# Optimization experiments

Hardware: AMD Instinct MI355X
Metric: run time of the kernel (lower is better)

Reference implementation:

```python
import jax, jax.numpy as jnp
import numpy as np

B, IN, H = 4096, 1024, 1024


def setup_inputs() -> dict:
    key = jax.random.key(0)
    ks = jax.random.split(key, 16)
    s_in = 1.0 / np.sqrt(IN)
    s_h = 1.0 / np.sqrt(H)
    d = {
        "x_t": jax.random.normal(ks[0], (B, IN), jnp.float32),
        "h_prev": jax.random.normal(ks[1], (B, H), jnp.float32),
        "c_prev": jax.random.normal(ks[2], (B, H), jnp.float32),
    }
    # input->hidden weights (with bias), stored torch-style as (out, in)
    for i, name in enumerate(["ii", "if", "ig", "io"]):
        d[f"W_{name}"] = jax.random.uniform(ks[3 + i], (H, IN), jnp.float32, -s_in, s_in)
        d[f"b_{name}"] = jax.random.uniform(ks[7 + i], (H,), jnp.float32, -s_in, s_in)
    # hidden->hidden weights (no bias)
    for i, name in enumerate(["hi", "hf", "hg", "ho"]):
        d[f"W_{name}"] = jax.random.uniform(ks[11 + i], (H, H), jnp.float32, -s_h, s_h)
    return d


def reference(x_t, h_prev, c_prev,
              W_ii, b_ii, W_if, b_if, W_ig, b_ig, W_io, b_io,
              W_hi, W_hf, W_hg, W_ho):
    # Fuse the 8 small GEMMs into 2 concatenated GEMMs (same math).
    Wx = jnp.concatenate([W_ii, W_if, W_ig, W_io], axis=0)   # (4H, IN)
    Wh = jnp.concatenate([W_hi, W_hf, W_hg, W_ho], axis=0)   # (4H, H)
    b = jnp.concatenate([b_ii, b_if, b_ig, b_io], axis=0)    # (4H,)
    gates = x_t @ Wx.T + h_prev @ Wh.T + b                    # (B, 4H)
    zi, zf, zg, zo = jnp.split(gates, 4, axis=1)
    i_t = jax.nn.sigmoid(zi)
    f_t = jax.nn.sigmoid(zf)
    g_t = jnp.tanh(zg)
    o_t = jax.nn.sigmoid(zo)
    c_t = f_t * c_prev + i_t * g_t
    h_t = o_t * jnp.tanh(c_t)
    return (h_t, c_t, (i_t, f_t, g_t, o_t))
```

## Files before the change

### kernel.cpp

```cpp
#include <hip/hip_runtime.h>
#include <hip/hip_bf16.h>

#define B_DIM 4096
#define K_TOT 2048
#define H_DIM 1024

typedef short bf16x8 __attribute__((ext_vector_type(8)));
typedef float f32x4 __attribute__((ext_vector_type(4)));
typedef unsigned short u16x8 __attribute__((ext_vector_type(8)));

typedef __attribute__((address_space(1))) const unsigned gas_u32;
typedef __attribute__((address_space(3))) unsigned las_u32;

static __device__ __forceinline__ unsigned short f2bf(float f) {
  union { float f; unsigned u; } v; v.f = f;
  unsigned r = v.u + 0x7FFF + ((v.u >> 16) & 1);
  return (unsigned short)(r >> 16);
}

__global__ void pack_a(const float* __restrict__ x, const float* __restrict__ hp,
                       u16x8* __restrict__ A) {
  int t = blockIdx.x * blockDim.x + threadIdx.x;
  int idx = t << 3;
  int b = idx >> 11;
  int k = idx & 2047;
  const float* src = (k < 1024) ? (x + b * 1024 + k) : (hp + b * 1024 + (k - 1024));
  float4 lo = *(const float4*)src;
  float4 hi = *(const float4*)(src + 4);
  u16x8 v;
  v[0] = f2bf(lo.x); v[1] = f2bf(lo.y); v[2] = f2bf(lo.z); v[3] = f2bf(lo.w);
  v[4] = f2bf(hi.x); v[5] = f2bf(hi.y); v[6] = f2bf(hi.z); v[7] = f2bf(hi.w);
  A[t] = v;
}

__global__ void pack_w(const float* __restrict__ W0, const float* __restrict__ W1,
                       const float* __restrict__ W2, const float* __restrict__ W3,
                       const float* __restrict__ W4, const float* __restrict__ W5,
                       const float* __restrict__ W6, const float* __restrict__ W7,
                       u16x8* __restrict__ Wc) {
  int t = blockIdx.x * blockDim.x + threadIdx.x;
  int idx = t << 3;
  int n = idx >> 11;
  int k = idx & 2047;
  int gate = n >> 10;
  int j = n & 1023;
  int s = (k < 1024) ? gate : gate + 4;
  const float* base =
      (s == 0) ? W0 : (s == 1) ? W1 : (s == 2) ? W2 : (s == 3) ? W3 :
      (s == 4) ? W4 : (s == 5) ? W5 : (s == 6) ? W6 : W7;
  const float* src = base + j * 1024 + (k & 1023);
  float4 lo = *(const float4*)src;
  float4 hi = *(const float4*)(src + 4);
  u16x8 v;
  v[0] = f2bf(lo.x); v[1] = f2bf(lo.y); v[2] = f2bf(lo.z); v[3] = f2bf(lo.w);
  v[4] = f2bf(hi.x); v[5] = f2bf(hi.y); v[6] = f2bf(hi.z); v[7] = f2bf(hi.w);
  Wc[t] = v;
}

static __device__ __forceinline__ float sigm(float x) {
  return 1.0f / (1.0f + __expf(-x));
}
static __device__ __forceinline__ float tanh_fast(float x) {
  x = fminf(fmaxf(x, -15.f), 15.f);
  float t = __expf(-2.0f * x);
  return (1.0f - t) / (1.0f + t);
}

__global__ __launch_bounds__(256) void gemm_lstm(
    const unsigned short* __restrict__ A,
    const unsigned short* __restrict__ W,
    const float* __restrict__ cp,
    const float* __restrict__ bii, const float* __restrict__ bif,
    const float* __restrict__ big, const float* __restrict__ bio,
    float* __restrict__ out) {
  __shared__ unsigned short As[128 * 32];
  __shared__ unsigned short Bs[128 * 32];
  const int tid = threadIdx.x;
  const int wave = tid >> 6;
  const int lane = tid & 63;
  const int m0 = blockIdx.y << 7;
  const int j0 = blockIdx.x << 5;
  const int wm = (wave >> 1) << 6;
  const int wj16 = (wave & 1) << 4;

  f32x4 acc[4][4];
#pragma unroll
  for (int mi = 0; mi < 4; ++mi)
#pragma unroll
    for (int ni = 0; ni < 4; ++ni)
      acc[mi][ni] = (f32x4){0.f, 0.f, 0.f, 0.f};

  const int c0 = wave * 2;
  const int lr = lane >> 2;
  const int ls = lane & 3;
  const int g  = ls ^ ((lr >> 1) & 3);
  const unsigned short* aptr0 = A + (long)(m0 + c0 * 16 + lr) * K_TOT + g * 8;
  const unsigned short* aptr1 = A + (long)(m0 + (c0 + 1) * 16 + lr) * K_TOT + g * 8;
  const int rr0 = c0 * 16 + lr;
  const int rr1 = rr0 + 16;
  const unsigned short* bptr0 =
      W + (long)((rr0 >> 5) * 1024 + j0 + (rr0 & 31)) * K_TOT + g * 8;
  const unsigned short* bptr1 =
      W + (long)((rr1 >> 5) * 1024 + j0 + (rr1 & 31)) * K_TOT + g * 8;
  char* lA0 = (char*)As + c0 * 1024;
  char* lA1 = lA0 + 1024;
  char* lB0 = (char*)Bs + c0 * 1024;
  char* lB1 = lB0 + 1024;

  const int fr = lane & 15;
  const int gg = lane >> 4;
  const int sl = (gg ^ ((fr >> 1) & 3)) * 16;

  for (int k0 = 0; k0 < K_TOT; k0 += 32) {
    __builtin_amdgcn_global_load_lds((gas_u32*)(aptr0 + k0), (las_u32*)lA0, 16, 0, 0);
    __builtin_amdgcn_global_load_lds((gas_u32*)(aptr1 + k0), (las_u32*)lA1, 16, 0, 0);
    __builtin_amdgcn_global_load_lds((gas_u32*)(bptr0 + k0), (las_u32*)lB0, 16, 0, 0);
    __builtin_amdgcn_global_load_lds((gas_u32*)(bptr1 + k0), (las_u32*)lB1, 16, 0, 0);
    __syncthreads();
    bf16x8 af[4], bfv[4];
#pragma unroll
    for (int i = 0; i < 4; ++i) {
      af[i]  = *(const bf16x8*)((const char*)As + (wm + i * 16 + fr) * 64 + sl);
      bfv[i] = *(const bf16x8*)((const char*)Bs + (i * 32 + wj16 + fr) * 64 + sl);
    }
#pragma unroll
    for (int mi = 0; mi < 4; ++mi)
#pragma unroll
      for (int ni = 0; ni < 4; ++ni)
        acc[mi][ni] = __builtin_amdgcn_mfma_f32_16x16x32_bf16(af[mi], bfv[ni], acc[mi][ni], 0, 0, 0);
    __syncthreads();
  }

  const int ccol = lane & 15;
  const int crow = (lane >> 4) * 4;
  const int j = j0 + wj16 + ccol;
  const float bi = bii[j];
  const float bff = bif[j];
  const float bg = big[j];
  const float bo = bio[j];
  const long BH = (long)B_DIM * H_DIM;
#pragma unroll
  for (int mi = 0; mi < 4; ++mi) {
#pragma unroll
    for (int reg = 0; reg < 4; ++reg) {
      const int row = m0 + wm + mi * 16 + crow + reg;
      const long p = (long)row * H_DIM + j;
      const float cvp = cp[p];
      const float iv = sigm(acc[mi][0][reg] + bi);
      const float fv = sigm(acc[mi][1][reg] + bff);
      const float gv = tanh_fast(acc[mi][2][reg] + bg);
      const float ov = sigm(acc[mi][3][reg] + bo);
      const float cv = fv * cvp + iv * gv;
      const float hv = ov * tanh_fast(cv);
      out[p]          = hv;
      out[BH + p]     = cv;
      out[2 * BH + p] = iv;
      out[3 * BH + p] = fv;
      out[4 * BH + p] = gv;
      out[5 * BH + p] = ov;
    }
  }
}

extern "C" void kernel_launch(void* const* d_in, const int* in_sizes, int n_in,
                              void* d_out, int out_size, void* d_ws, size_t ws_size,
                              hipStream_t stream) {
  const float* x    = (const float*)d_in[0];
  const float* h    = (const float*)d_in[1];
  const float* c    = (const float*)d_in[2];
  const float* W_ii = (const float*)d_in[3];
  const float* b_ii = (const float*)d_in[4];
  const float* W_if = (const float*)d_in[5];
  const float* b_if = (const float*)d_in[6];
  const float* W_ig = (const float*)d_in[7];
  const float* b_ig = (const float*)d_in[8];
  const float* W_io = (const float*)d_in[9];
  const float* b_io = (const float*)d_in[10];
  const float* W_hi = (const float*)d_in[11];
  const float* W_hf = (const float*)d_in[12];
  const float* W_hg = (const float*)d_in[13];
  const float* W_ho = (const float*)d_in[14];

  unsigned short* Abf = (unsigned short*)d_ws;
  unsigned short* Wbf = (unsigned short*)((char*)d_ws + (size_t)16 * 1024 * 1024);

  pack_a<<<4096, 256, 0, stream>>>(x, h, (u16x8*)Abf);
  pack_w<<<4096, 256, 0, stream>>>(W_ii, W_if, W_ig, W_io, W_hi, W_hf, W_hg, W_ho,
                                   (u16x8*)Wbf);
  dim3 grid(H_DIM / 32, B_DIM / 128);
  gemm_lstm<<<grid, 256, 0, stream>>>(Abf, Wbf, c, b_ii, b_if, b_ig, b_io,
                                      (float*)d_out);
}
```

Before: 282.5 us.

## Merge pack kernels and shrink GEMM tile to 64 rows with two waves

Merges the separate activation and weight bf16 packing kernels into one launch, removing one kernel launch and its serialization gap. It also cuts the GEMM block tile from 128x128 to 64x128 (128 threads, 2 waves, each wave covering all 64 rows and a 16-column slice of each gate), doubling the grid to raise block count and occupancy. The cost is lower reuse of each weight tile loaded into LDS, so more global/L2 traffic per output, plus more per-wave B loads.

```diff
diff --git a/kernel.cpp b/kernel.cpp
--- a/kernel.cpp
+++ b/kernel.cpp
@@ -18,43 +18,43 @@
   return (unsigned short)(r >> 16);
 }
 
-__global__ void pack_a(const float* __restrict__ x, const float* __restrict__ hp,
-                       u16x8* __restrict__ A) {
-  int t = blockIdx.x * blockDim.x + threadIdx.x;
-  int idx = t << 3;
-  int b = idx >> 11;
-  int k = idx & 2047;
-  const float* src = (k < 1024) ? (x + b * 1024 + k) : (hp + b * 1024 + (k - 1024));
+__global__ void pack_all(const float* __restrict__ x, const float* __restrict__ hp,
+                         const float* __restrict__ W0, const float* __restrict__ W1,
+                         const float* __restrict__ W2, const float* __restrict__ W3,
+                         const float* __restrict__ W4, const float* __restrict__ W5,
+                         const float* __restrict__ W6, const float* __restrict__ W7,
+                         u16x8* __restrict__ A, u16x8* __restrict__ Wc) {
+  int blk = blockIdx.x;
+  const float* src;
+  u16x8* dst;
+  int t;
+  if (blk < 4096) {
+    t = blk * blockDim.x + threadIdx.x;
+    int idx = t << 3;
+    int b = idx >> 11;
+    int k = idx & 2047;
+    src = (k < 1024) ? (x + b * 1024 + k) : (hp + b * 1024 + (k - 1024));
+    dst = A + t;
+  } else {
+    t = (blk - 4096) * blockDim.x + threadIdx.x;
+    int idx = t << 3;
+    int n = idx >> 11;
+    int k = idx & 2047;
+    int gate = n >> 10;
+    int j = n & 1023;
+    int s = (k < 1024) ? gate : gate + 4;
+    const float* base =
+        (s == 0) ? W0 : (s == 1) ? W1 : (s == 2) ? W2 : (s == 3) ? W3 :
+        (s == 4) ? W4 : (s == 5) ? W5 : (s == 6) ? W6 : W7;
+    src = base + j * 1024 + (k & 1023);
+    dst = Wc + t;
+  }
   float4 lo = *(const float4*)src;
   float4 hi = *(const float4*)(src + 4);
   u16x8 v;
   v[0] = f2bf(lo.x); v[1] = f2bf(lo.y); v[2] = f2bf(lo.z); v[3] = f2bf(lo.w);
   v[4] = f2bf(hi.x); v[5] = f2bf(hi.y); v[6] = f2bf(hi.z); v[7] = f2bf(hi.w);
-  A[t] = v;
-}
-
-__global__ void pack_w(const float* __restrict__ W0, const float* __restrict__ W1,
-                       const float* __restrict__ W2, const float* __restrict__ W3,
-                       const float* __restrict__ W4, const float* __restrict__ W5,
-                       const float* __restrict__ W6, const float* __restrict__ W7,
-                       u16x8* __restrict__ Wc) {
-  int t = blockIdx.x * blockDim.x + threadIdx.x;
-  int idx = t << 3;
-  int n = idx >> 11;
-  int k = idx & 2047;
-  int gate = n >> 10;
-  int j = n & 1023;
-  int s = (k < 1024) ? gate : gate + 4;
-  const float* base =
-      (s == 0) ? W0 : (s == 1) ? W1 : (s == 2) ? W2 : (s == 3) ? W3 :
-      (s == 4) ? W4 : (s == 5) ? W5 : (s == 6) ? W6 : W7;
-  const float* src = base + j * 1024 + (k & 1023);
-  float4 lo = *(const float4*)src;
-  float4 hi = *(const float4*)(src + 4);
-  u16x8 v;
-  v[0] = f2bf(lo.x); v[1] = f2bf(lo.y); v[2] = f2bf(lo.z); v[3] = f2bf(lo.w);
-  v[4] = f2bf(hi.x); v[5] = f2bf(hi.y); v[6] = f2bf(hi.z); v[7] = f2bf(hi.w);
-  Wc[t] = v;
+  *dst = v;
 }
 
 static __device__ __forceinline__ float sigm(float x) {
@@ -66,22 +66,21 @@
   return (1.0f - t) / (1.0f + t);
 }
 
-__global__ __launch_bounds__(256) void gemm_lstm(
+__global__ __launch_bounds__(128) void gemm_lstm(
     const unsigned short* __restrict__ A,
     const unsigned short* __restrict__ W,
     const float* __restrict__ cp,
     const float* __restrict__ bii, const float* __restrict__ bif,
     const float* __restrict__ big, const float* __restrict__ bio,
     float* __restrict__ out) {
-  __shared__ unsigned short As[128 * 32];
+  __shared__ unsigned short As[64 * 32];
   __shared__ unsigned short Bs[128 * 32];
   const int tid = threadIdx.x;
   const int wave = tid >> 6;
   const int lane = tid & 63;
-  const int m0 = blockIdx.y << 7;
+  const int m0 = blockIdx.y << 6;
   const int j0 = blockIdx.x << 5;
-  const int wm = (wave >> 1) << 6;
-  const int wj16 = (wave & 1) << 4;
+  const int wj16 = wave << 4;
 
   f32x4 acc[4][4];
 #pragma unroll
@@ -90,22 +89,25 @@
     for (int ni = 0; ni < 4; ++ni)
       acc[mi][ni] = (f32x4){0.f, 0.f, 0.f, 0.f};
 
-  const int c0 = wave * 2;
   const int lr = lane >> 2;
   const int ls = lane & 3;
   const int g  = ls ^ ((lr >> 1) & 3);
-  const unsigned short* aptr0 = A + (long)(m0 + c0 * 16 + lr) * K_TOT + g * 8;
-  const unsigned short* aptr1 = A + (long)(m0 + (c0 + 1) * 16 + lr) * K_TOT + g * 8;
-  const int rr0 = c0 * 16 + lr;
-  const int rr1 = rr0 + 16;
-  const unsigned short* bptr0 =
-      W + (long)((rr0 >> 5) * 1024 + j0 + (rr0 & 31)) * K_TOT + g * 8;
-  const unsigned short* bptr1 =
-      W + (long)((rr1 >> 5) * 1024 + j0 + (rr1 & 31)) * K_TOT + g * 8;
-  char* lA0 = (char*)As + c0 * 1024;
+
+  const int ca = wave * 2;
+  const unsigned short* aptr0 = A + (long)(m0 + ca * 16 + lr) * K_TOT + g * 8;
+  const unsigned short* aptr1 = A + (long)(m0 + (ca + 1) * 16 + lr) * K_TOT + g * 8;
+  char* lA0 = (char*)As + ca * 1024;
   char* lA1 = lA0 + 1024;
-  char* lB0 = (char*)Bs + c0 * 1024;
-  char* lB1 = lB0 + 1024;
+
+  const int cb = wave * 4;
+  const unsigned short* bptr[4];
+  char* lB[4];
+#pragma unroll
+  for (int q = 0; q < 4; ++q) {
+    int rr = (cb + q) * 16 + lr;
+    bptr[q] = W + (long)((rr >> 5) * 1024 + j0 + (rr & 31)) * K_TOT + g * 8;
+    lB[q] = (char*)Bs + (cb + q) * 1024;
+  }
 
   const int fr = lane & 15;
   const int gg = lane >> 4;
@@ -114,13 +116,14 @@
   for (int k0 = 0; k0 < K_TOT; k0 += 32) {
     __builtin_amdgcn_global_load_lds((gas_u32*)(aptr0 + k0), (las_u32*)lA0, 16, 0, 0);
     __builtin_amdgcn_global_load_lds((gas_u32*)(aptr1 + k0), (las_u32*)lA1, 16, 0, 0);
-    __builtin_amdgcn_global_load_lds((gas_u32*)(bptr0 + k0), (las_u32*)lB0, 16, 0, 0);
-    __builtin_amdgcn_global_load_lds((gas_u32*)(bptr1 + k0), (las_u32*)lB1, 16, 0, 0);
+#pragma unroll
+    for (int q = 0; q < 4; ++q)
+      __builtin_amdgcn_global_load_lds((gas_u32*)(bptr[q] + k0), (las_u32*)lB[q], 16, 0, 0);
     __syncthreads();
     bf16x8 af[4], bfv[4];
 #pragma unroll
     for (int i = 0; i < 4; ++i) {
-      af[i]  = *(const bf16x8*)((const char*)As + (wm + i * 16 + fr) * 64 + sl);
+      af[i]  = *(const bf16x8*)((const char*)As + (i * 16 + fr) * 64 + sl);
       bfv[i] = *(const bf16x8*)((const char*)Bs + (i * 32 + wj16 + fr) * 64 + sl);
     }
 #pragma unroll
@@ -143,7 +146,7 @@
   for (int mi = 0; mi < 4; ++mi) {
 #pragma unroll
     for (int reg = 0; reg < 4; ++reg) {
-      const int row = m0 + wm + mi * 16 + crow + reg;
+      const int row = m0 + mi * 16 + crow + reg;
       const long p = (long)row * H_DIM + j;
       const float cvp = cp[p];
       const float iv = sigm(acc[mi][0][reg] + bi);
@@ -184,10 +187,10 @@
   unsigned short* Abf = (unsigned short*)d_ws;
   unsigned short* Wbf = (unsigned short*)((char*)d_ws + (size_t)16 * 1024 * 1024);
 
-  pack_a<<<4096, 256, 0, stream>>>(x, h, (u16x8*)Abf);
-  pack_w<<<4096, 256, 0, stream>>>(W_ii, W_if, W_ig, W_io, W_hi, W_hf, W_hg, W_ho,
-                                   (u16x8*)Wbf);
-  dim3 grid(H_DIM / 32, B_DIM / 128);
-  gemm_lstm<<<grid, 256, 0, stream>>>(Abf, Wbf, c, b_ii, b_if, b_ig, b_io,
+  pack_all<<<8192, 256, 0, stream>>>(x, h, W_ii, W_if, W_ig, W_io,
+                                     W_hi, W_hf, W_hg, W_ho,
+                                     (u16x8*)Abf, (u16x8*)Wbf);
+  dim3 grid(H_DIM / 32, B_DIM / 64);
+  gemm_lstm<<<grid, 128, 0, stream>>>(Abf, Wbf, c, b_ii, b_if, b_ig, b_io,
                                       (float*)d_out);
 }
```

After: 316.6 us. 1.12x slower.
